# Optimization experiments

Measured on AMD Instinct MI355X. Metric: run time of the kernel, lower is better.

Reference implementation:

```python
import jax, jax.numpy as jnp
import numpy as np
import math

B, S, E, H = 2, 4096, 1024, 1024

def setup_inputs() -> dict:
    key = jax.random.key(0)
    ks = jax.random.split(key, 7)
    X = jax.random.normal(ks[0], (B, S, E), dtype=jnp.float32)
    attention_mask = jnp.ones((B, S, S), dtype=jnp.int32)
    sc = 1.0 / math.sqrt(E)
    Wq = jax.random.normal(ks[1], (H, E), dtype=jnp.float32) * sc
    Wk = jax.random.normal(ks[2], (H, E), dtype=jnp.float32) * sc
    Wv = jax.random.normal(ks[3], (H, E), dtype=jnp.float32) * sc
    bq = jnp.zeros((H,), dtype=jnp.float32)
    bk = jnp.zeros((H,), dtype=jnp.float32)
    bv = jnp.zeros((H,), dtype=jnp.float32)
    return {"X": X, "attention_mask": attention_mask,
            "Wq": Wq, "bq": bq, "Wk": Wk, "bk": bk, "Wv": Wv, "bv": bv}

def reference(X, attention_mask, Wq, bq, Wk, bk, Wv, bv):
    # Linear layers: y = x @ W^T + b (torch convention W is [out, in])
    Q = jnp.einsum('bse,he->bsh', X, Wq) + bq
    K = jnp.einsum('bse,he->bsh', X, Wk) + bk
    V = jnp.einsum('bse,he->bsh', X, Wv) + bv
    scale = 1.0 / math.sqrt(H)
    scores = jnp.einsum('bqh,bkh->bqk', Q, K) * scale  # [B,S,S]
    scores = jnp.where(attention_mask == 0, -jnp.inf, scores)
    # dropout (eval mode -> identity) would be applied here, BEFORE softmax
    weights = jax.nn.softmax(scores, axis=-1)
    out = jnp.einsum('bqk,bkh->bqh', weights, V)  # [B,S,H]
    return out
```

## Files before the change

kernel.cpp:

```cpp
#include <hip/hip_runtime.h>
#include <stdint.h>


typedef __bf16 bf16;
typedef __attribute__((ext_vector_type(4))) __bf16 bf16x4;
typedef __attribute__((ext_vector_type(8))) __bf16 bf16x8;
typedef __attribute__((ext_vector_type(4))) float f32x4;

__device__ __forceinline__ void g2l16(const void* g, void* l) {
  __builtin_amdgcn_global_load_lds(
      (const __attribute__((address_space(1))) uint32_t*)g,
      (__attribute__((address_space(3))) uint32_t*)l, 16, 0, 0);
}

__global__ __launch_bounds__(256) void cvt_f32_bf16(
    const float* __restrict__ src, bf16* __restrict__ dst, int n) {
  const int i = (blockIdx.x * 256 + threadIdx.x) * 8;
  if (i >= n) return;
  f32x4 a = *(const f32x4*)(src + i);
  f32x4 b = *(const f32x4*)(src + i + 4);
  bf16x8 o;
#pragma unroll
  for (int e = 0; e < 4; ++e) { o[e] = (bf16)a[e]; o[4 + e] = (bf16)b[e]; }
  *(bf16x8*)(dst + i) = o;
}

__global__ __launch_bounds__(256) void cvt_w3(
    const float* __restrict__ Wq, const float* __restrict__ Wk,
    const float* __restrict__ Wv, bf16* __restrict__ dst) {
  const int i = (blockIdx.x * 256 + threadIdx.x) * 8;
  const int seg = i >> 20;
  const int off = i & 1048575;
  const float* src = (seg == 0) ? Wq : (seg == 1) ? Wk : Wv;
  f32x4 a = *(const f32x4*)(src + off);
  f32x4 b = *(const f32x4*)(src + off + 4);
  bf16x8 o;
#pragma unroll
  for (int e = 0; e < 4; ++e) { o[e] = (bf16)a[e]; o[4 + e] = (bf16)b[e]; }
  *(bf16x8*)(dst + i) = o;
}


__global__ __launch_bounds__(256, 2) void gemm_qkv(
    const bf16* __restrict__ Xb, const bf16* __restrict__ Wb3,
    const float* __restrict__ bq, const float* __restrict__ bk,
    const float* __restrict__ bv, bf16* __restrict__ QK,
    bf16* __restrict__ Vt)
{
  constexpr int K = 1024, N = 1024;
  __shared__ __align__(16) bf16 ldsA[128 * 64];
  __shared__ __align__(16) bf16 ldsB[128 * 64];

  const int tid  = threadIdx.x;
  const int lane = tid & 63;
  const int wave = tid >> 6;
  const int which = blockIdx.y >> 3;
  const int n0 = (blockIdx.y & 7) * 128;
  const int m0 = blockIdx.x * 128;
  const bf16* Bt = Wb3 + (size_t)which * 1048576;
  const float* bias = (which == 0) ? bq : ((which == 1) ? bk : bv);

  const int l15  = lane & 15;
  const int quad = lane >> 4;
  const int wm = (wave >> 1) * 64;
  const int wn = (wave & 1) * 64;
  const int sw = l15 & 7;

  f32x4 acc[4][4];
#pragma unroll
  for (int i = 0; i < 4; ++i)
#pragma unroll
    for (int j = 0; j < 4; ++j) acc[i][j] = f32x4{0.f, 0.f, 0.f, 0.f};

  const int srow = tid >> 3;
  const int scol = ((tid & 7) ^ (srow & 7)) * 8;
  const size_t a_base = (size_t)(m0 + srow) * K + scol;
  const size_t b_base = (size_t)(n0 + srow) * K + scol;
  const int lds_off = tid * 8;

  for (int kt = 0; kt < K; kt += 64) {
    const bf16* ga = Xb + a_base + kt;
    const bf16* gb = Bt + b_base + kt;
#pragma unroll
    for (int it = 0; it < 4; ++it) {
      g2l16(ga + (size_t)(it * 32) * K, &ldsA[lds_off + it * 2048]);
      g2l16(gb + (size_t)(it * 32) * K, &ldsB[lds_off + it * 2048]);
    }
    __syncthreads();
#pragma unroll
    for (int ks = 0; ks < 2; ++ks) {
      const int ch = ks * 4 + quad;
      bf16x8 af[4], bfg[4];
#pragma unroll
      for (int i = 0; i < 4; ++i)
        af[i] = *(const bf16x8*)&ldsA[(wm + i * 16 + l15) * 64 + (ch ^ sw) * 8];
#pragma unroll
      for (int j = 0; j < 4; ++j)
        bfg[j] = *(const bf16x8*)&ldsB[(wn + j * 16 + l15) * 64 + (ch ^ sw) * 8];
#pragma unroll
      for (int i = 0; i < 4; ++i)
#pragma unroll
        for (int j = 0; j < 4; ++j)
          acc[i][j] = __builtin_amdgcn_mfma_f32_16x16x32_bf16(
              af[i], bfg[j], acc[i][j], 0, 0, 0);
    }
    __syncthreads();
  }

  if (which < 2) {
    bf16* C = QK + (size_t)which * (size_t)(8192 * 1024);
#pragma unroll
    for (int i = 0; i < 4; ++i) {
#pragma unroll
      for (int j = 0; j < 4; ++j) {
        const int r = m0 + wm + i * 16 + quad * 4;
        const int c = n0 + wn + j * 16 + l15;
        const float bvv = bias[c];
        f32x4 v = acc[i][j];
#pragma unroll
        for (int reg = 0; reg < 4; ++reg)
          C[(size_t)(r + reg) * N + c] = (bf16)(v[reg] + bvv);
      }
    }
  } else {
#pragma unroll
    for (int i = 0; i < 4; ++i) {
#pragma unroll
      for (int j = 0; j < 4; ++j) {
        const int r = m0 + wm + i * 16 + quad * 4;
        const int c = n0 + wn + j * 16 + l15;
        const int b = r >> 12, s = r & 4095;
        const float bvv = bias[c];
        f32x4 v = acc[i][j];
        bf16x4 o;
#pragma unroll
        for (int reg = 0; reg < 4; ++reg) o[reg] = (bf16)(v[reg] + bvv);
        *(bf16x4*)&Vt[((size_t)(b * 1024 + c)) * 4096 + s] = o;
      }
    }
  }
}

__global__ __launch_bounds__(256, 2) void gemm_scores(
    const bf16* __restrict__ A, const bf16* __restrict__ Bt,
    const int* __restrict__ mask, bf16* __restrict__ P,
    float* __restrict__ row_sum)
{
  constexpr int N = 4096, K = 1024;
  __shared__ __align__(16) bf16 ldsA[128 * 64];
  __shared__ __align__(16) bf16 ldsB[128 * 64];

  const int tid  = threadIdx.x;
  const int lane = tid & 63;
  const int wave = tid >> 6;
  const int m0 = blockIdx.x * 128;
  const int n0 = blockIdx.y * 128;
  const int batch = m0 >> 12;
  const bf16* Btb = Bt + (size_t)batch * (size_t)(4096 * 1024);

  const int l15  = lane & 15;
  const int quad = lane >> 4;
  const int wm = (wave >> 1) * 64;
  const int wn = (wave & 1) * 64;
  const int sw = l15 & 7;

  f32x4 acc[4][4];
#pragma unroll
  for (int i = 0; i < 4; ++i)
#pragma unroll
    for (int j = 0; j < 4; ++j) acc[i][j] = f32x4{0.f, 0.f, 0.f, 0.f};

  const int srow = tid >> 3;
  const int scol = ((tid & 7) ^ (srow & 7)) * 8;
  const size_t a_base = (size_t)(m0 + srow) * K + scol;
  const size_t b_base = (size_t)(n0 + srow) * K + scol;
  const int lds_off = tid * 8;

  for (int kt = 0; kt < K; kt += 64) {
    const bf16* ga = A + a_base + kt;
    const bf16* gb = Btb + b_base + kt;
#pragma unroll
    for (int it = 0; it < 4; ++it) {
      g2l16(ga + (size_t)(it * 32) * K, &ldsA[lds_off + it * 2048]);
      g2l16(gb + (size_t)(it * 32) * K, &ldsB[lds_off + it * 2048]);
    }
    __syncthreads();
#pragma unroll
    for (int ks = 0; ks < 2; ++ks) {
      const int ch = ks * 4 + quad;
      bf16x8 af[4], bfg[4];
#pragma unroll
      for (int i = 0; i < 4; ++i)
        af[i] = *(const bf16x8*)&ldsA[(wm + i * 16 + l15) * 64 + (ch ^ sw) * 8];
#pragma unroll
      for (int j = 0; j < 4; ++j)
        bfg[j] = *(const bf16x8*)&ldsB[(wn + j * 16 + l15) * 64 + (ch ^ sw) * 8];
#pragma unroll
      for (int i = 0; i < 4; ++i)
#pragma unroll
        for (int j = 0; j < 4; ++j)
          acc[i][j] = __builtin_amdgcn_mfma_f32_16x16x32_bf16(
              af[i], bfg[j], acc[i][j], 0, 0, 0);
    }
    __syncthreads();
  }

#pragma unroll
  for (int i = 0; i < 4; ++i) {
    const int r = m0 + wm + i * 16 + quad * 4;
    f32x4 rsum = f32x4{0.f, 0.f, 0.f, 0.f};
#pragma unroll
    for (int j = 0; j < 4; ++j) {
      const int c = n0 + wn + j * 16 + l15;
      f32x4 v = acc[i][j];
#pragma unroll
      for (int reg = 0; reg < 4; ++reg) {
        float e = __expf(v[reg] * 0.03125f);
        if (mask[(size_t)(r + reg) * N + c] == 0) e = 0.f;
        P[(size_t)(r + reg) * N + c] = (bf16)e;
        rsum[reg] += e;
      }
    }
#pragma unroll
    for (int off = 1; off < 16; off <<= 1) {
#pragma unroll
      for (int reg = 0; reg < 4; ++reg)
        rsum[reg] += __shfl_xor(rsum[reg], off);
    }
    if (l15 == 0) {
#pragma unroll
      for (int reg = 0; reg < 4; ++reg)
        atomicAdd(&row_sum[r + reg], rsum[reg]);
    }
  }
}

__global__ __launch_bounds__(256, 2) void gemm_pv(
    const bf16* __restrict__ A, const bf16* __restrict__ Bt,
    const float* __restrict__ row_sum, float* __restrict__ C)
{
  constexpr int N = 1024, K = 4096;
  __shared__ __align__(16) bf16 ldsA[128 * 64];
  __shared__ __align__(16) bf16 ldsB[128 * 64];

  const int tid  = threadIdx.x;
  const int lane = tid & 63;
  const int wave = tid >> 6;
  const int m0 = blockIdx.x * 128;
  const int n0 = blockIdx.y * 128;
  const int batch = m0 >> 12;
  const bf16* Btb = Bt + (size_t)batch * (size_t)(1024 * 4096);

  const int l15  = lane & 15;
  const int quad = lane >> 4;
  const int wm = (wave >> 1) * 64;
  const int wn = (wave & 1) * 64;
  const int sw = l15 & 7;

  f32x4 acc[4][4];
#pragma unroll
  for (int i = 0; i < 4; ++i)
#pragma unroll
    for (int j = 0; j < 4; ++j) acc[i][j] = f32x4{0.f, 0.f, 0.f, 0.f};

  const int srow = tid >> 3;
  const int scol = ((tid & 7) ^ (srow & 7)) * 8;
  const size_t a_base = (size_t)(m0 + srow) * K + scol;
  const size_t b_base = (size_t)(n0 + srow) * K + scol;
  const int lds_off = tid * 8;

  for (int kt = 0; kt < K; kt += 64) {
    const bf16* ga = A + a_base + kt;
    const bf16* gb = Btb + b_base + kt;
#pragma unroll
    for (int it = 0; it < 4; ++it) {
      g2l16(ga + (size_t)(it * 32) * K, &ldsA[lds_off + it * 2048]);
      g2l16(gb + (size_t)(it * 32) * K, &ldsB[lds_off + it * 2048]);
    }
    __syncthreads();
#pragma unroll
    for (int ks = 0; ks < 2; ++ks) {
      const int ch = ks * 4 + quad;
      bf16x8 af[4], bfg[4];
#pragma unroll
      for (int i = 0; i < 4; ++i)
        af[i] = *(const bf16x8*)&ldsA[(wm + i * 16 + l15) * 64 + (ch ^ sw) * 8];
#pragma unroll
      for (int j = 0; j < 4; ++j)
        bfg[j] = *(const bf16x8*)&ldsB[(wn + j * 16 + l15) * 64 + (ch ^ sw) * 8];
#pragma unroll
      for (int i = 0; i < 4; ++i)
#pragma unroll
        for (int j = 0; j < 4; ++j)
          acc[i][j] = __builtin_amdgcn_mfma_f32_16x16x32_bf16(
              af[i], bfg[j], acc[i][j], 0, 0, 0);
    }
    __syncthreads();
  }

#pragma unroll
  for (int i = 0; i < 4; ++i) {
    const int r = m0 + wm + i * 16 + quad * 4;
    f32x4 inv;
#pragma unroll
    for (int reg = 0; reg < 4; ++reg) inv[reg] = 1.0f / row_sum[r + reg];
#pragma unroll
    for (int j = 0; j < 4; ++j) {
      const int c = n0 + wn + j * 16 + l15;
      f32x4 v = acc[i][j];
#pragma unroll
      for (int reg = 0; reg < 4; ++reg)
        C[(size_t)(r + reg) * N + c] = v[reg] * inv[reg];
    }
  }
}

extern "C" void kernel_launch(void* const* d_in, const int* in_sizes, int n_in,
                              void* d_out, int out_size, void* d_ws,
                              size_t ws_size, hipStream_t stream) {
  const float* X   = (const float*)d_in[0];
  const int* mask  = (const int*)d_in[1];
  const float* Wq  = (const float*)d_in[2];
  const float* bq  = (const float*)d_in[3];
  const float* Wk  = (const float*)d_in[4];
  const float* bk  = (const float*)d_in[5];
  const float* Wv  = (const float*)d_in[6];
  const float* bv  = (const float*)d_in[7];
  float* out = (float*)d_out;

  const size_t QKV_ELEMS = (size_t)8192 * 1024;
  bf16* Q    = (bf16*)d_ws;
  bf16* Kb   = Q + QKV_ELEMS;
  bf16* X_bf = Kb + QKV_ELEMS;
  bf16* Vt   = X_bf + QKV_ELEMS;
  bf16* Sc   = Vt + QKV_ELEMS;
  bf16* W_bf = Sc;
  float* row_sum = (float*)X_bf;

  const dim3 blk(256);
  cvt_f32_bf16<<<dim3(4096), blk, 0, stream>>>(X, X_bf, 8388608);
  cvt_w3<<<dim3(1536), blk, 0, stream>>>(Wq, Wk, Wv, W_bf);
  gemm_qkv<<<dim3(64, 24), blk, 0, stream>>>(X_bf, W_bf, bq, bk, bv, Q, Vt);
  hipMemsetAsync(row_sum, 0, 8192 * sizeof(float), stream);
  gemm_scores<<<dim3(64, 32), blk, 0, stream>>>(Q, Kb, mask, Sc, row_sum);
  gemm_pv<<<dim3(64, 8), blk, 0, stream>>>(Sc, Vt, row_sum, out);
}
```

Baseline: 427.4 us.

## Pack attention mask into bitmask in fused prep kernel

Merges the X and weight conversion kernels into a single prep launch. That launch also packs the int32 attention mask into a 1-bit-per-element bitmask, staged in the output buffer. gemm_scores then reads one 64-bit word per row segment instead of scattered int32 mask loads in its epilogue. The goal is to replace the strided 128MB mask reads inside the scores epilogue with a coalesced streaming pass plus a 4MB bitmask. The full mask still has to be read once, and the output buffer is reused as scratch before gemm_pv overwrites it.

```diff
diff --git a/kernel.cpp b/kernel.cpp
--- a/kernel.cpp
+++ b/kernel.cpp
@@ -6,6 +6,7 @@
 typedef __attribute__((ext_vector_type(4))) __bf16 bf16x4;
 typedef __attribute__((ext_vector_type(8))) __bf16 bf16x8;
 typedef __attribute__((ext_vector_type(4))) float f32x4;
+typedef __attribute__((ext_vector_type(4))) int i32x4;
 
 __device__ __forceinline__ void g2l16(const void* g, void* l) {
   __builtin_amdgcn_global_load_lds(
@@ -13,31 +14,45 @@
       (__attribute__((address_space(3))) uint32_t*)l, 16, 0, 0);
 }
 
-__global__ __launch_bounds__(256) void cvt_f32_bf16(
-    const float* __restrict__ src, bf16* __restrict__ dst, int n) {
-  const int i = (blockIdx.x * 256 + threadIdx.x) * 8;
-  if (i >= n) return;
-  f32x4 a = *(const f32x4*)(src + i);
-  f32x4 b = *(const f32x4*)(src + i + 4);
-  bf16x8 o;
-#pragma unroll
-  for (int e = 0; e < 4; ++e) { o[e] = (bf16)a[e]; o[4 + e] = (bf16)b[e]; }
-  *(bf16x8*)(dst + i) = o;
-}
-
-__global__ __launch_bounds__(256) void cvt_w3(
-    const float* __restrict__ Wq, const float* __restrict__ Wk,
-    const float* __restrict__ Wv, bf16* __restrict__ dst) {
-  const int i = (blockIdx.x * 256 + threadIdx.x) * 8;
-  const int seg = i >> 20;
-  const int off = i & 1048575;
-  const float* src = (seg == 0) ? Wq : (seg == 1) ? Wk : Wv;
-  f32x4 a = *(const f32x4*)(src + off);
-  f32x4 b = *(const f32x4*)(src + off + 4);
-  bf16x8 o;
-#pragma unroll
-  for (int e = 0; e < 4; ++e) { o[e] = (bf16)a[e]; o[4 + e] = (bf16)b[e]; }
-  *(bf16x8*)(dst + i) = o;
+__global__ __launch_bounds__(256) void prep(
+    const float* __restrict__ X, const float* __restrict__ Wq,
+    const float* __restrict__ Wk, const float* __restrict__ Wv,
+    const int* __restrict__ mask, bf16* __restrict__ X_bf,
+    bf16* __restrict__ W_bf, uint32_t* __restrict__ mbits)
+{
+  const int b = blockIdx.x;
+  if (b < 4096) {
+    const int i = (b * 256 + threadIdx.x) * 8;
+    f32x4 a = *(const f32x4*)(X + i);
+    f32x4 c = *(const f32x4*)(X + i + 4);
+    bf16x8 o;
+#pragma unroll
+    for (int e = 0; e < 4; ++e) { o[e] = (bf16)a[e]; o[4 + e] = (bf16)c[e]; }
+    *(bf16x8*)(X_bf + i) = o;
+  } else if (b < 5632) {
+    const int i = ((b - 4096) * 256 + threadIdx.x) * 8;
+    const int seg = i >> 20;
+    const int off = i & 1048575;
+    const float* src = (seg == 0) ? Wq : (seg == 1) ? Wk : Wv;
+    f32x4 a = *(const f32x4*)(src + off);
+    f32x4 c = *(const f32x4*)(src + off + 4);
+    bf16x8 o;
+#pragma unroll
+    for (int e = 0; e < 4; ++e) { o[e] = (bf16)a[e]; o[4 + e] = (bf16)c[e]; }
+    *(bf16x8*)(W_bf + i) = o;
+  } else {
+    const int t = (b - 5632) * 256 + threadIdx.x;
+    const int* p = mask + (size_t)t * 32;
+    uint32_t w = 0;
+#pragma unroll
+    for (int ch = 0; ch < 8; ++ch) {
+      i32x4 v = *(const i32x4*)(p + ch * 4);
+#pragma unroll
+      for (int e = 0; e < 4; ++e)
+        if (v[e] != 0) w |= 1u << (ch * 4 + e);
+    }
+    mbits[t] = w;
+  }
 }
 
 
@@ -143,7 +158,7 @@
 
 __global__ __launch_bounds__(256, 2) void gemm_scores(
     const bf16* __restrict__ A, const bf16* __restrict__ Bt,
-    const int* __restrict__ mask, bf16* __restrict__ P,
+    const uint64_t* __restrict__ mb, bf16* __restrict__ P,
     float* __restrict__ row_sum)
 {
   constexpr int N = 4096, K = 1024;
@@ -207,7 +222,11 @@
 
 #pragma unroll
   for (int i = 0; i < 4; ++i) {
-    const int r = m0 + wm + i * 16 + quad * 4;
+    const int rb = m0 + wm + i * 16 + quad * 4;
+    uint64_t w[4];
+#pragma unroll
+    for (int reg = 0; reg < 4; ++reg)
+      w[reg] = mb[((size_t)(rb + reg) * N + (n0 + wn)) >> 6];
     f32x4 rsum = f32x4{0.f, 0.f, 0.f, 0.f};
 #pragma unroll
     for (int j = 0; j < 4; ++j) {
@@ -216,8 +235,8 @@
 #pragma unroll
       for (int reg = 0; reg < 4; ++reg) {
         float e = __expf(v[reg] * 0.03125f);
-        if (mask[(size_t)(r + reg) * N + c] == 0) e = 0.f;
-        P[(size_t)(r + reg) * N + c] = (bf16)e;
+        if (!((w[reg] >> (j * 16 + l15)) & 1)) e = 0.f;
+        P[(size_t)(rb + reg) * N + c] = (bf16)e;
         rsum[reg] += e;
       }
     }
@@ -230,7 +249,7 @@
     if (l15 == 0) {
 #pragma unroll
       for (int reg = 0; reg < 4; ++reg)
-        atomicAdd(&row_sum[r + reg], rsum[reg]);
+        atomicAdd(&row_sum[rb + reg], rsum[reg]);
     }
   }
 }
@@ -336,12 +355,13 @@
   bf16* Sc   = Vt + QKV_ELEMS;
   bf16* W_bf = Sc;
   float* row_sum = (float*)X_bf;
+  uint32_t* mbits = (uint32_t*)d_out;
 
   const dim3 blk(256);
-  cvt_f32_bf16<<<dim3(4096), blk, 0, stream>>>(X, X_bf, 8388608);
-  cvt_w3<<<dim3(1536), blk, 0, stream>>>(Wq, Wk, Wv, W_bf);
+  prep<<<dim3(9728), blk, 0, stream>>>(X, Wq, Wk, Wv, mask, X_bf, W_bf, mbits);
   gemm_qkv<<<dim3(64, 24), blk, 0, stream>>>(X_bf, W_bf, bq, bk, bv, Q, Vt);
   hipMemsetAsync(row_sum, 0, 8192 * sizeof(float), stream);
-  gemm_scores<<<dim3(64, 32), blk, 0, stream>>>(Q, Kb, mask, Sc, row_sum);
+  gemm_scores<<<dim3(64, 32), blk, 0, stream>>>(
+      Q, Kb, (const uint64_t*)mbits, Sc, row_sum);
   gemm_pv<<<dim3(64, 8), blk, 0, stream>>>(Sc, Vt, row_sum, out);
 }
```

Result: slower. 446.5 us (+4.5%).
